# Kernel optimization log

Measured on AMD Instinct MI355X. Metric: run time of the kernel, lower is better.

## Reference

```python
import jax, jax.numpy as jnp
import numpy as np


def setup_inputs() -> dict:
    key = jax.random.key(0)
    k1, k2 = jax.random.split(key)
    B, H, W, C = 8, 32, 32, 512
    N = 25000
    feature_batch = jax.random.normal(k1, (B, H, W, C), dtype=jnp.float32)
    mb = jax.random.normal(k2, (N, C), dtype=jnp.float32)
    return {"feature_batch": feature_batch, "mb": mb, "b": 9}


def reference(feature_batch, mb, b):
    # feature_batch: (B,H,W,C), mb: (N,C), b: python int
    B, H, W, C = feature_batch.shape
    fv = feature_batch.reshape(B * H * W, C)
    sq_dists = ((fv * fv).sum(1)[:, None]
                + (mb * mb).sum(1)[None, :]
                - 2.0 * fv @ mb.T)                      # (BHW, N)
    pixel_scores = jnp.sqrt(sq_dists.min(axis=1)).reshape(B, H * W)
    # index of most anomalous pixel per image
    idx = jnp.argmax(pixel_scores, axis=1)              # (B,)
    flat_idx = idx + jnp.arange(B) * (H * W)
    selected = fv[flat_idx]                             # (B, C)
    # exact squared distances of selected vectors to full memory bank
    dists_to_mb = ((selected[:, None, :] - mb[None, :, :]) ** 2).sum(-1)  # (B, N)
    # b nearest memory-bank entries (ascending distance order)
    _, b_closest_idx = jax.lax.top_k(-dists_to_mb, b)   # (B, b)
    sel_mb = mb[b_closest_idx]                          # (B, b, C)
    selected_dists = jnp.sqrt(((selected[:, None, :] - sel_mb) ** 2).sum(-1))  # (B, b)
    image_scores = selected_dists[:, 0]
    if b > 1:
        image_scores = image_scores * (1.0 - jax.nn.softmax(selected_dists, axis=1)[:, 0])
    return pixel_scores.reshape(B, 1, H, W), image_scores
```

## Files before the change

### kernel.cpp

```cpp
#include <hip/hip_runtime.h>
#include <hip/hip_bf16.h>

typedef __attribute__((ext_vector_type(8))) short short8;
typedef __attribute__((ext_vector_type(4))) float f32x4;

#define INF_F 3.4e38f

__device__ __forceinline__ void gload16(const void* g, void* l) {
    __builtin_amdgcn_global_load_lds((const __attribute__((address_space(1))) unsigned*)g,
                                     (__attribute__((address_space(3))) unsigned*)l, 16, 0, 0);
}

__global__ void k_conv(const float* __restrict__ fv, const float* __restrict__ mbp,
                       unsigned short* __restrict__ fvb, unsigned short* __restrict__ mbb,
                       float* __restrict__ fnorm, float* __restrict__ mnorm,
                       float* ps_sq, int* ncand, float* cand_val) {
    int t = threadIdx.x, wid = t >> 6, lane = t & 63;
    if (blockIdx.x == 0) {
        if (t == 0) ncand[0] = 0;
        if (t < 64) ((unsigned*)cand_val)[t] = 0x7f800000u;
    }
    int row = blockIdx.x * 4 + wid;
    const float* in; unsigned short* outb; float* norm; int r;
    if (row < 8192) {
        in = fv; outb = fvb; norm = fnorm; r = row;
        if (lane == 0) ((unsigned*)ps_sq)[row] = 0x7f800000u;
    } else if (row < 33192) {
        in = mbp; outb = mbb; norm = mnorm; r = row - 8192;
    } else return;
    const float4* p = (const float4*)(in + (size_t)r * 512) + lane * 2;
    float4 a = p[0], b = p[1];
    float n = a.x*a.x + a.y*a.y + a.z*a.z + a.w*a.w
            + b.x*b.x + b.y*b.y + b.z*b.z + b.w*b.w;
    float vals[8] = {a.x, a.y, a.z, a.w, b.x, b.y, b.z, b.w};
    unsigned short h[8];
    #pragma unroll
    for (int e = 0; e < 8; ++e) {
        unsigned u = __float_as_uint(vals[e]);
        h[e] = (unsigned short)((u + 0x7fffu + ((u >> 16) & 1u)) >> 16);
    }
    *(uint4*)(outb + (size_t)r * 512 + lane * 8) = *(uint4*)h;
    #pragma unroll
    for (int s = 1; s < 64; s <<= 1) n += __shfl_xor(n, s, 64);
    if (lane == 0) norm[r] = n;
}

__global__ __launch_bounds__(256, 2)
void k_gemm_min(const unsigned short* __restrict__ A, const unsigned short* __restrict__ B,
                const float* __restrict__ fnorm, const float* __restrict__ mnorm,
                float* __restrict__ ps_sq) {
    __shared__ unsigned short At[128 * 64];
    __shared__ unsigned short Bt[128 * 64];
    int tid = threadIdx.x, wid = tid >> 6, lane = tid & 63;
    int bid = blockIdx.x;
    int pos = bid >> 3;
    int rb = ((bid & 7) << 3) | (pos & 7);
    int cb = pos >> 3;
    int brow = rb * 128, bcol = cb * 128;
    int wm = (wid >> 1) * 64, wn = (wid & 1) * 64;

    f32x4 acc[4][4] = {};
    int lr = lane >> 3;
    int lkswz = ((lane & 7) ^ lr) * 8;

    for (int k0 = 0; k0 < 512; k0 += 64) {
        #pragma unroll
        for (int c = 0; c < 4; ++c) {
            int ch = wid + c * 4;
            int row = ch * 8 + lr;
            gload16(A + (size_t)(brow + row) * 512 + k0 + lkswz, &At[ch * 512]);
            int srow = bcol + row; if (srow > 24999) srow = 24999;
            gload16(B + (size_t)srow * 512 + k0 + lkswz, &Bt[ch * 512]);
        }
        __syncthreads();
        #pragma unroll
        for (int kk = 0; kk < 2; ++kk) {
            short8 af[4], bf[4];
            int ko = kk * 32 + (lane >> 4) * 8;
            #pragma unroll
            for (int mi = 0; mi < 4; ++mi) {
                int r = wm + mi * 16 + (lane & 15);
                af[mi] = *(const short8*)&At[r * 64 + (ko ^ ((r & 7) << 3))];
            }
            #pragma unroll
            for (int ni = 0; ni < 4; ++ni) {
                int r = wn + ni * 16 + (lane & 15);
                bf[ni] = *(const short8*)&Bt[r * 64 + (ko ^ ((r & 7) << 3))];
            }
            #pragma unroll
            for (int mi = 0; mi < 4; ++mi)
                #pragma unroll
                for (int ni = 0; ni < 4; ++ni)
                    acc[mi][ni] = __builtin_amdgcn_mfma_f32_16x16x32_bf16(af[mi], bf[ni], acc[mi][ni], 0, 0, 0);
        }
        __syncthreads();
    }

    float mnv[4];
    #pragma unroll
    for (int ni = 0; ni < 4; ++ni) {
        int col = bcol + wn + ni * 16 + (lane & 15);
        mnv[ni] = (col < 25000) ? mnorm[col] : INF_F;
    }
    #pragma unroll
    for (int mi = 0; mi < 4; ++mi) {
        #pragma unroll
        for (int r = 0; r < 4; ++r) {
            float v = INF_F;
            #pragma unroll
            for (int ni = 0; ni < 4; ++ni) v = fminf(v, mnv[ni] - 2.0f * acc[mi][ni][r]);
            #pragma unroll
            for (int s = 1; s < 16; s <<= 1) v = fminf(v, __shfl_xor(v, s, 64));
            if ((lane & 15) == 0) {
                int row = brow + wm + mi * 16 + (lane >> 4) * 4 + r;
                float sq = v + fnorm[row];
                atomicMin((unsigned*)&ps_sq[row], __float_as_uint(sq));
            }
        }
    }
}

__global__ void k_cand(const float* __restrict__ ps_sq, float* __restrict__ out0,
                       int* ncand, int* cand_pix, int* cand_batch) {
    __shared__ float smax[4];
    __shared__ int scnt;
    int b = blockIdx.x, t = threadIdx.x, wid = t >> 6, lane = t & 63;
    const float* base = ps_sq + b * 1024;
    float v[4]; float m = -INF_F;
    #pragma unroll
    for (int i = 0; i < 4; ++i) {
        v[i] = base[t + i * 256];
        out0[b * 1024 + t + i * 256] = sqrtf(fmaxf(v[i], 0.0f));
        m = fmaxf(m, v[i]);
    }
    #pragma unroll
    for (int s = 1; s < 64; s <<= 1) m = fmaxf(m, __shfl_xor(m, s, 64));
    if (lane == 0) smax[wid] = m;
    if (t == 0) scnt = 0;
    __syncthreads();
    float bm = fmaxf(fmaxf(smax[0], smax[1]), fmaxf(smax[2], smax[3]));
    #pragma unroll
    for (int i = 0; i < 4; ++i) {
        if (v[i] >= bm - 8.0f) {
            int s = atomicAdd(&scnt, 1);
            if (s < 8) {
                int g = atomicAdd(ncand, 1);
                if (g < 64) { cand_pix[g] = b * 1024 + t + i * 256; cand_batch[g] = b; }
            }
        }
    }
}

__global__ __launch_bounds__(256, 4)
void k_score(const float* __restrict__ fv, const float* __restrict__ mb,
             const int* __restrict__ ncand, const int* __restrict__ cand_pix,
             float* __restrict__ cand_val) {
    int nct = ncand[0]; if (nct > 64) nct = 64;
    int c0 = blockIdx.y * 4;
    if (c0 >= nct) return;
    int t = threadIdx.x, wid = t >> 6, lane = t & 63;

    int p0i = cand_pix[c0];
    int p1i = cand_pix[c0 + 1 < nct ? c0 + 1 : c0];
    int p2i = cand_pix[c0 + 2 < nct ? c0 + 2 : c0];
    int p3i = cand_pix[c0 + 3 < nct ? c0 + 3 : c0];
    const float4* s0 = (const float4*)(fv + (size_t)p0i * 512) + lane * 2;
    const float4* s1 = (const float4*)(fv + (size_t)p1i * 512) + lane * 2;
    const float4* s2 = (const float4*)(fv + (size_t)p2i * 512) + lane * 2;
    const float4* s3 = (const float4*)(fv + (size_t)p3i * 512) + lane * 2;
    float4 ca0 = s0[0], ca1 = s0[1];
    float4 cb0 = s1[0], cb1 = s1[1];
    float4 cc0 = s2[0], cc1 = s2[1];
    float4 cd0 = s3[0], cd1 = s3[1];

    float m0v = INF_F, m1v = INF_F, m2v = INF_F, m3v = INF_F;
    int rbase = blockIdx.x * 64 + wid * 16;
    for (int i = 0; i < 16; ++i) {
        int r = rbase + i;
        if (r >= 25000) break;
        const float4* mp = (const float4*)(mb + (size_t)r * 512) + lane * 2;
        float4 x0 = mp[0], x1 = mp[1];
        float d, p0 = 0.f, p1 = 0.f, p2 = 0.f, p3 = 0.f;
        d = x0.x-ca0.x; p0 += d*d;  d = x0.y-ca0.y; p0 += d*d;  d = x0.z-ca0.z; p0 += d*d;  d = x0.w-ca0.w; p0 += d*d;
        d = x1.x-ca1.x; p0 += d*d;  d = x1.y-ca1.y; p0 += d*d;  d = x1.z-ca1.z; p0 += d*d;  d = x1.w-ca1.w; p0 += d*d;
        d = x0.x-cb0.x; p1 += d*d;  d = x0.y-cb0.y; p1 += d*d;  d = x0.z-cb0.z; p1 += d*d;  d = x0.w-cb0.w; p1 += d*d;
        d = x1.x-cb1.x; p1 += d*d;  d = x1.y-cb1.y; p1 += d*d;  d = x1.z-cb1.z; p1 += d*d;  d = x1.w-cb1.w; p1 += d*d;
        d = x0.x-cc0.x; p2 += d*d;  d = x0.y-cc0.y; p2 += d*d;  d = x0.z-cc0.z; p2 += d*d;  d = x0.w-cc0.w; p2 += d*d;
        d = x1.x-cc1.x; p2 += d*d;  d = x1.y-cc1.y; p2 += d*d;  d = x1.z-cc1.z; p2 += d*d;  d = x1.w-cc1.w; p2 += d*d;
        d = x0.x-cd0.x; p3 += d*d;  d = x0.y-cd0.y; p3 += d*d;  d = x0.z-cd0.z; p3 += d*d;  d = x0.w-cd0.w; p3 += d*d;
        d = x1.x-cd1.x; p3 += d*d;  d = x1.y-cd1.y; p3 += d*d;  d = x1.z-cd1.z; p3 += d*d;  d = x1.w-cd1.w; p3 += d*d;
        #pragma unroll
        for (int s = 1; s < 64; s <<= 1) {
            p0 += __shfl_xor(p0, s, 64);
            p1 += __shfl_xor(p1, s, 64);
            p2 += __shfl_xor(p2, s, 64);
            p3 += __shfl_xor(p3, s, 64);
        }
        m0v = fminf(m0v, p0); m1v = fminf(m1v, p1);
        m2v = fminf(m2v, p2); m3v = fminf(m3v, p3);
    }
    if (lane < 4 && c0 + lane < nct) {
        float mv = (lane == 0) ? m0v : (lane == 1) ? m1v : (lane == 2) ? m2v : m3v;
        atomicMin((unsigned*)&cand_val[c0 + lane], __float_as_uint(mv));
    }
}

__global__ void k_argmax(const int* ncand, const int* cand_pix, const int* cand_batch,
                         const float* cand_val, int* sel_pix) {
    int b = blockIdx.x, lane = threadIdx.x;
    int n = ncand[0]; if (n > 64) n = 64;
    float v = -INF_F; int pix = 0x7fffffff;
    if (lane < n && cand_batch[lane] == b) { v = cand_val[lane]; pix = cand_pix[lane]; }
    #pragma unroll
    for (int s = 1; s < 64; s <<= 1) {
        float ov = __shfl_xor(v, s, 64); int oi = __shfl_xor(pix, s, 64);
        if (ov > v || (ov == v && oi < pix)) { v = ov; pix = oi; }
    }
    if (lane == 0) sel_pix[b] = (pix == 0x7fffffff) ? b * 1024 : pix;
}

__global__ __launch_bounds__(256, 4)
void k_dists4(const float* __restrict__ fv, const float* __restrict__ mb,
              const int* __restrict__ sel_pix, float* __restrict__ exact_d) {
    int bg = blockIdx.y * 4;
    int t = threadIdx.x, wid = t >> 6, lane = t & 63;

    const float4* s0 = (const float4*)(fv + (size_t)sel_pix[bg + 0] * 512) + lane * 2;
    const float4* s1 = (const float4*)(fv + (size_t)sel_pix[bg + 1] * 512) + lane * 2;
    const float4* s2 = (const float4*)(fv + (size_t)sel_pix[bg + 2] * 512) + lane * 2;
    const float4* s3 = (const float4*)(fv + (size_t)sel_pix[bg + 3] * 512) + lane * 2;
    float4 ca0 = s0[0], ca1 = s0[1];
    float4 cb0 = s1[0], cb1 = s1[1];
    float4 cc0 = s2[0], cc1 = s2[1];
    float4 cd0 = s3[0], cd1 = s3[1];

    int rbase = blockIdx.x * 64 + wid * 16;
    for (int i = 0; i < 16; ++i) {
        int r = rbase + i;
        if (r >= 25000) break;
        const float4* mp = (const float4*)(mb + (size_t)r * 512) + lane * 2;
        float4 x0 = mp[0], x1 = mp[1];
        float d, p0 = 0.f, p1 = 0.f, p2 = 0.f, p3 = 0.f;
        d = x0.x-ca0.x; p0 += d*d;  d = x0.y-ca0.y; p0 += d*d;  d = x0.z-ca0.z; p0 += d*d;  d = x0.w-ca0.w; p0 += d*d;
        d = x1.x-ca1.x; p0 += d*d;  d = x1.y-ca1.y; p0 += d*d;  d = x1.z-ca1.z; p0 += d*d;  d = x1.w-ca1.w; p0 += d*d;
        d = x0.x-cb0.x; p1 += d*d;  d = x0.y-cb0.y; p1 += d*d;  d = x0.z-cb0.z; p1 += d*d;  d = x0.w-cb0.w; p1 += d*d;
        d = x1.x-cb1.x; p1 += d*d;  d = x1.y-cb1.y; p1 += d*d;  d = x1.z-cb1.z; p1 += d*d;  d = x1.w-cb1.w; p1 += d*d;
        d = x0.x-cc0.x; p2 += d*d;  d = x0.y-cc0.y; p2 += d*d;  d = x0.z-cc0.z; p2 += d*d;  d = x0.w-cc0.w; p2 += d*d;
        d = x1.x-cc1.x; p2 += d*d;  d = x1.y-cc1.y; p2 += d*d;  d = x1.z-cc1.z; p2 += d*d;  d = x1.w-cc1.w; p2 += d*d;
        d = x0.x-cd0.x; p3 += d*d;  d = x0.y-cd0.y; p3 += d*d;  d = x0.z-cd0.z; p3 += d*d;  d = x0.w-cd0.w; p3 += d*d;
        d = x1.x-cd1.x; p3 += d*d;  d = x1.y-cd1.y; p3 += d*d;  d = x1.z-cd1.z; p3 += d*d;  d = x1.w-cd1.w; p3 += d*d;
        #pragma unroll
        for (int s = 1; s < 64; s <<= 1) {
            p0 += __shfl_xor(p0, s, 64);
            p1 += __shfl_xor(p1, s, 64);
            p2 += __shfl_xor(p2, s, 64);
            p3 += __shfl_xor(p3, s, 64);
        }
        if (lane < 4) {
            float pv = (lane == 0) ? p0 : (lane == 1) ? p1 : (lane == 2) ? p2 : p3;
            exact_d[(size_t)(bg + lane) * 25000 + r] = pv;
        }
    }
}

__global__ __launch_bounds__(1024)
void k_final(const float* __restrict__ exact_d, const int* __restrict__ bptr,
             float* __restrict__ out_img) {
    __shared__ float rv[16]; __shared__ int ri[16];
    __shared__ float seld[128];
    __shared__ float lastV_s; __shared__ int lastI_s;
    int b = blockIdx.x, t = threadIdx.x, wid = t >> 6, lane = t & 63;
    int bval = bptr[0]; if (bval > 128) bval = 128; if (bval < 1) bval = 1;
    const float* dv = exact_d + (size_t)b * 25000;
    float lastV = -INF_F; int lastI = -1;
    for (int k = 0; k < bval; ++k) {
        float bv = INF_F; int bi = 0x7fffffff;
        for (int r = t; r < 25000; r += 1024) {
            float vv = dv[r];
            bool after = (vv > lastV) || (vv == lastV && r > lastI);
            if (after && (vv < bv || (vv == bv && r < bi))) { bv = vv; bi = r; }
        }
        #pragma unroll
        for (int s = 1; s < 64; s <<= 1) {
            float ov = __shfl_xor(bv, s, 64); int oi = __shfl_xor(bi, s, 64);
            if (ov < bv || (ov == bv && oi < bi)) { bv = ov; bi = oi; }
        }
        if (lane == 0) { rv[wid] = bv; ri[wid] = bi; }
        __syncthreads();
        if (t == 0) {
            float fbv = rv[0]; int fbi = ri[0];
            for (int w = 1; w < 16; ++w)
                if (rv[w] < fbv || (rv[w] == fbv && ri[w] < fbi)) { fbv = rv[w]; fbi = ri[w]; }
            seld[k] = sqrtf(fbv);
            lastV_s = fbv; lastI_s = fbi;
        }
        __syncthreads();
        lastV = lastV_s; lastI = lastI_s;
    }
    if (t == 0) {
        float d0 = seld[0];
        float img = d0;
        if (bval > 1) {
            float m = -INF_F;
            for (int k = 0; k < bval; ++k) m = fmaxf(m, seld[k]);
            float s = 0.f;
            for (int k = 0; k < bval; ++k) s += expf(seld[k] - m);
            float p0 = expf(seld[0] - m) / s;
            img = d0 * (1.0f - p0);
        }
        out_img[b] = img;
    }
}

extern "C" void kernel_launch(void* const* d_in, const int* in_sizes, int n_in,
                              void* d_out, int out_size, void* d_ws, size_t ws_size,
                              hipStream_t stream) {
    const float* fv = (const float*)d_in[0];
    const float* mb = (const float*)d_in[1];
    const int*   bp = (const int*)d_in[2];
    float* out = (float*)d_out;

    char* w = (char*)d_ws;
    unsigned short* fvb = (unsigned short*)w;
    unsigned short* mbb = (unsigned short*)(w + 8388608);
    size_t o = 8388608 + 25600000;
    float* fnorm    = (float*)(w + o); o += 32768;
    float* mnorm    = (float*)(w + o); o += 100352;
    float* ps_sq    = (float*)(w + o); o += 32768;
    int*   ncand    = (int*)(w + o);   o += 256;
    int*   cand_pix = (int*)(w + o);   o += 256;
    int*   cand_bat = (int*)(w + o);   o += 256;
    float* cand_val = (float*)(w + o); o += 256;
    int*   sel_pix  = (int*)(w + o);   o += 256;
    float* exact_d  = (float*)(w + o); o += 800000;

    k_conv<<<8298, 256, 0, stream>>>(fv, mb, fvb, mbb, fnorm, mnorm, ps_sq, ncand, cand_val);
    k_gemm_min<<<12544, 256, 0, stream>>>(fvb, mbb, fnorm, mnorm, ps_sq);
    k_cand<<<8, 256, 0, stream>>>(ps_sq, out, ncand, cand_pix, cand_bat);
    k_score<<<dim3(391, 16), 256, 0, stream>>>(fv, mb, ncand, cand_pix, cand_val);
    k_argmax<<<8, 64, 0, stream>>>(ncand, cand_pix, cand_bat, cand_val, sel_pix);
    k_dists4<<<dim3(391, 2), 256, 0, stream>>>(fv, mb, sel_pix, exact_d);
    k_final<<<8, 1024, 0, stream>>>(exact_d, bp, out + 8192);
}
```

Before: 472.6 us.

## Use 256x256 tiles with double-buffered LDS pipeline in distance GEMM

Rewrites the bf16 distance GEMM to use 256x256 block tiles with 512 threads (8 waves, each 128x64). K-slices are double-buffered in 128KB of LDS, with async global-to-LDS loads interleaved between MFMA phases, vmcnt-based waits and s_setprio around the MFMA bursts. The aim is to hide global load latency behind compute and to raise data reuse per tile. In exchange, the large LDS footprint and 128 accumulator registers per thread limit occupancy, and there are fewer blocks to spread across the CUs.

Result: slower. 545.9 us (+15.5%).

```diff
diff --git a/kernel.cpp b/kernel.cpp
--- a/kernel.cpp
+++ b/kernel.cpp
@@ -10,6 +10,11 @@
     __builtin_amdgcn_global_load_lds((const __attribute__((address_space(1))) unsigned*)g,
                                      (__attribute__((address_space(3))) unsigned*)l, 16, 0, 0);
 }
+
+#define SBAR() do { __builtin_amdgcn_s_barrier(); __builtin_amdgcn_sched_barrier(0); } while(0)
+#define VMCNT4() asm volatile("s_waitcnt vmcnt(4)" ::: "memory")
+#define VMCNT0() asm volatile("s_waitcnt vmcnt(0)" ::: "memory")
+#define MF(a,b,cc) __builtin_amdgcn_mfma_f32_16x16x32_bf16((a),(b),(cc),0,0,0)
 
 __global__ void k_conv(const float* __restrict__ fv, const float* __restrict__ mbp,
                        unsigned short* __restrict__ fvb, unsigned short* __restrict__ mbb,
@@ -45,74 +50,103 @@
     if (lane == 0) norm[r] = n;
 }
 
-__global__ __launch_bounds__(256, 2)
+__global__ __launch_bounds__(512, 2)
 void k_gemm_min(const unsigned short* __restrict__ A, const unsigned short* __restrict__ B,
                 const float* __restrict__ fnorm, const float* __restrict__ mnorm,
                 float* __restrict__ ps_sq) {
-    __shared__ unsigned short At[128 * 64];
-    __shared__ unsigned short Bt[128 * 64];
+    __shared__ unsigned short sh[65536];
     int tid = threadIdx.x, wid = tid >> 6, lane = tid & 63;
-    int bid = blockIdx.x;
-    int pos = bid >> 3;
-    int rb = ((bid & 7) << 3) | (pos & 7);
-    int cb = pos >> 3;
-    int brow = rb * 128, bcol = cb * 128;
-    int wm = (wid >> 1) * 64, wn = (wid & 1) * 64;
-
-    f32x4 acc[4][4] = {};
-    int lr = lane >> 3;
-    int lkswz = ((lane & 7) ^ lr) * 8;
-
-    for (int k0 = 0; k0 < 512; k0 += 64) {
-        #pragma unroll
-        for (int c = 0; c < 4; ++c) {
-            int ch = wid + c * 4;
-            int row = ch * 8 + lr;
-            gload16(A + (size_t)(brow + row) * 512 + k0 + lkswz, &At[ch * 512]);
-            int srow = bcol + row; if (srow > 24999) srow = 24999;
-            gload16(B + (size_t)srow * 512 + k0 + lkswz, &Bt[ch * 512]);
-        }
-        __syncthreads();
-        #pragma unroll
-        for (int kk = 0; kk < 2; ++kk) {
-            short8 af[4], bf[4];
-            int ko = kk * 32 + (lane >> 4) * 8;
-            #pragma unroll
-            for (int mi = 0; mi < 4; ++mi) {
-                int r = wm + mi * 16 + (lane & 15);
-                af[mi] = *(const short8*)&At[r * 64 + (ko ^ ((r & 7) << 3))];
-            }
-            #pragma unroll
-            for (int ni = 0; ni < 4; ++ni) {
-                int r = wn + ni * 16 + (lane & 15);
-                bf[ni] = *(const short8*)&Bt[r * 64 + (ko ^ ((r & 7) << 3))];
-            }
-            #pragma unroll
-            for (int mi = 0; mi < 4; ++mi)
-                #pragma unroll
-                for (int ni = 0; ni < 4; ++ni)
-                    acc[mi][ni] = __builtin_amdgcn_mfma_f32_16x16x32_bf16(af[mi], bf[ni], acc[mi][ni], 0, 0, 0);
-        }
-        __syncthreads();
-    }
+    int l15 = lane & 15, c = lane >> 4;
+    int bid = blockIdx.x, pos = bid >> 3;
+    int rb = ((bid & 7) << 2) | (pos & 3);
+    int cb = pos >> 2;
+    int brow = rb * 256, bcol = cb * 256;
+    int wr = wid >> 2, wc = wid & 3;
+
+    int grow0, grow1, c80, c81;
+    { int i = tid;       int pr = i >> 3, gp = i & 7, g = gp ^ (pr & 7); grow0 = ((g >> 2) << 7) + pr; c80 = (g & 3) * 8; }
+    { int i = 512 + tid; int pr = i >> 3, gp = i & 7, g = gp ^ (pr & 7); grow1 = ((g >> 2) << 7) + pr; c81 = (g & 3) * 8; }
+    const unsigned short* gA0 = A + (size_t)(brow + grow0) * 512 + c80;
+    const unsigned short* gA1 = A + (size_t)(brow + grow1) * 512 + c81;
+    int sb0 = bcol + grow0; if (sb0 > 24999) sb0 = 24999;
+    int sb1 = bcol + grow1; if (sb1 > 24999) sb1 = 24999;
+    const unsigned short* gB0 = B + (size_t)sb0 * 512 + c80;
+    const unsigned short* gB1 = B + (size_t)sb1 * 512 + c81;
+
+#define STAGE_A(TT, KH, SLOT) do { \
+        gload16(gA0 + (TT)*64 + (KH)*32, sh + (SLOT)*32768 + (KH)*8192 + wid*512); \
+        gload16(gA1 + (TT)*64 + (KH)*32, sh + (SLOT)*32768 + (KH)*8192 + 4096 + wid*512); } while(0)
+#define STAGE_B(TT, KH, SLOT) do { \
+        gload16(gB0 + (TT)*64 + (KH)*32, sh + (SLOT)*32768 + 16384 + (KH)*8192 + wid*512); \
+        gload16(gB1 + (TT)*64 + (KH)*32, sh + (SLOT)*32768 + 16384 + (KH)*8192 + 4096 + wid*512); } while(0)
+#define FRAG(MOFF, KK, RV) (*(const short8*)&sh[cur*32768 + (MOFF) + (KK)*8192 + ((RV)&127)*64 + (((((RV)>>7)<<2)+c)^((RV)&7))*8])
+
+#define PHASE(QB, KK, LOADB, STAGES, TAIL) do { \
+        af0 = FRAG(0, KK, wr*128 + (QB+0)*16 + l15); \
+        af1 = FRAG(0, KK, wr*128 + (QB+1)*16 + l15); \
+        af2 = FRAG(0, KK, wr*128 + (QB+2)*16 + l15); \
+        af3 = FRAG(0, KK, wr*128 + (QB+3)*16 + l15); \
+        if (LOADB) { \
+            bf0 = FRAG(16384, KK, wc*64 +  0 + l15); \
+            bf1 = FRAG(16384, KK, wc*64 + 16 + l15); \
+            bf2 = FRAG(16384, KK, wc*64 + 32 + l15); \
+            bf3 = FRAG(16384, KK, wc*64 + 48 + l15); \
+        } \
+        STAGES; \
+        SBAR(); \
+        __builtin_amdgcn_s_setprio(1); \
+        acc[QB+0][0]=MF(af0,bf0,acc[QB+0][0]); acc[QB+0][1]=MF(af0,bf1,acc[QB+0][1]); \
+        acc[QB+0][2]=MF(af0,bf2,acc[QB+0][2]); acc[QB+0][3]=MF(af0,bf3,acc[QB+0][3]); \
+        acc[QB+1][0]=MF(af1,bf0,acc[QB+1][0]); acc[QB+1][1]=MF(af1,bf1,acc[QB+1][1]); \
+        acc[QB+1][2]=MF(af1,bf2,acc[QB+1][2]); acc[QB+1][3]=MF(af1,bf3,acc[QB+1][3]); \
+        acc[QB+2][0]=MF(af2,bf0,acc[QB+2][0]); acc[QB+2][1]=MF(af2,bf1,acc[QB+2][1]); \
+        acc[QB+2][2]=MF(af2,bf2,acc[QB+2][2]); acc[QB+2][3]=MF(af2,bf3,acc[QB+2][3]); \
+        acc[QB+3][0]=MF(af3,bf0,acc[QB+3][0]); acc[QB+3][1]=MF(af3,bf1,acc[QB+3][1]); \
+        acc[QB+3][2]=MF(af3,bf2,acc[QB+3][2]); acc[QB+3][3]=MF(af3,bf3,acc[QB+3][3]); \
+        __builtin_amdgcn_s_setprio(0); \
+        TAIL; \
+        SBAR(); \
+    } while(0)
+
+    f32x4 acc[8][4] = {};
+
+    STAGE_A(0, 0, 0); STAGE_B(0, 0, 0); STAGE_A(0, 1, 0); STAGE_B(0, 1, 0);
+    STAGE_A(1, 0, 1); STAGE_B(1, 0, 1);
+    VMCNT4();
+    SBAR();
+
+    #pragma unroll
+    for (int t = 0; t < 8; ++t) {
+        const int cur = t & 1, nxt = cur ^ 1;
+        short8 af0, af1, af2, af3, bf0, bf1, bf2, bf3;
+        PHASE(0, 0, 1, { if (t < 7) STAGE_A(t + 1, 1, nxt); }, {});
+        PHASE(4, 0, 0, { if (t < 7) STAGE_B(t + 1, 1, nxt); }, {});
+        PHASE(0, 1, 1, { if (t < 6) STAGE_A(t + 2, 0, cur); }, {});
+        PHASE(4, 1, 0, { if (t < 6) STAGE_B(t + 2, 0, cur); },
+              { if (t < 6) { VMCNT4(); } else if (t == 6) { VMCNT0(); } });
+    }
+#undef PHASE
+#undef FRAG
+#undef STAGE_A
+#undef STAGE_B
 
     float mnv[4];
     #pragma unroll
-    for (int ni = 0; ni < 4; ++ni) {
-        int col = bcol + wn + ni * 16 + (lane & 15);
-        mnv[ni] = (col < 25000) ? mnorm[col] : INF_F;
-    }
-    #pragma unroll
-    for (int mi = 0; mi < 4; ++mi) {
+    for (int n = 0; n < 4; ++n) {
+        int col = bcol + wc * 64 + n * 16 + l15;
+        mnv[n] = (col < 25000) ? mnorm[col] : INF_F;
+    }
+    #pragma unroll
+    for (int mi = 0; mi < 8; ++mi) {
         #pragma unroll
         for (int r = 0; r < 4; ++r) {
             float v = INF_F;
             #pragma unroll
-            for (int ni = 0; ni < 4; ++ni) v = fminf(v, mnv[ni] - 2.0f * acc[mi][ni][r]);
+            for (int n = 0; n < 4; ++n) v = fminf(v, mnv[n] - 2.0f * acc[mi][n][r]);
             #pragma unroll
             for (int s = 1; s < 16; s <<= 1) v = fminf(v, __shfl_xor(v, s, 64));
-            if ((lane & 15) == 0) {
-                int row = brow + wm + mi * 16 + (lane >> 4) * 4 + r;
+            if (l15 == 0) {
+                int row = brow + wr * 128 + mi * 16 + c * 4 + r;
                 float sq = v + fnorm[row];
                 atomicMin((unsigned*)&ps_sq[row], __float_as_uint(sq));
             }
@@ -335,7 +369,7 @@
     float* exact_d  = (float*)(w + o); o += 800000;
 
     k_conv<<<8298, 256, 0, stream>>>(fv, mb, fvb, mbb, fnorm, mnorm, ps_sq, ncand, cand_val);
-    k_gemm_min<<<12544, 256, 0, stream>>>(fvb, mbb, fnorm, mnorm, ps_sq);
+    k_gemm_min<<<3136, 512, 0, stream>>>(fvb, mbb, fnorm, mnorm, ps_sq);
     k_cand<<<8, 256, 0, stream>>>(ps_sq, out, ncand, cand_pix, cand_bat);
     k_score<<<dim3(391, 16), 256, 0, stream>>>(fv, mb, ncand, cand_pix, cand_val);
     k_argmax<<<8, 64, 0, stream>>>(ncand, cand_pix, cand_bat, cand_val, sel_pix);
```
